# Optimization experiments

Hardware: AMD Instinct MI355X
Metric: run time of the kernel (lower is better)

Reference implementation:

```python
import jax, jax.numpy as jnp
import numpy as np

C = 512
NUM_HEADS = 8
GROUPS = 32
EPS_GN = 1e-5
EPS_ATTN = 1e-6


def setup_inputs() -> dict:
    key = jax.random.key(0)
    ks = jax.random.split(key, 7)
    B, H, W = 8, 64, 64
    x = jax.random.normal(ks[0], (B, C, H, W), dtype=jnp.float32)
    # GroupNorm affine (torch default: weight=1, bias=0)
    norm_gamma = jnp.ones((C,), dtype=jnp.float32)
    norm_beta = jnp.zeros((C,), dtype=jnp.float32)
    # 1x1 conv weights stored as (out, in); torch Conv2d kaiming-ish scale
    qkv_w = jax.random.normal(ks[1], (3 * C, C), dtype=jnp.float32) * (1.0 / np.sqrt(C))
    qkv_b = jax.random.normal(ks[2], (3 * C,), dtype=jnp.float32) * 0.01
    proj_w = jax.random.normal(ks[3], (C, C), dtype=jnp.float32) * (1.0 / np.sqrt(C))
    proj_b = jax.random.normal(ks[4], (C,), dtype=jnp.float32) * 0.01
    return {"x": x, "norm_gamma": norm_gamma, "norm_beta": norm_beta,
            "qkv_w": qkv_w, "qkv_b": qkv_b, "proj_w": proj_w, "proj_b": proj_b}


def _group_norm(x, gamma, beta):
    B, Cc, H, W = x.shape
    xg = x.reshape(B, GROUPS, Cc // GROUPS, H, W)
    mean = xg.mean(axis=(2, 3, 4), keepdims=True)
    var = xg.var(axis=(2, 3, 4), keepdims=True)
    xn = (xg - mean) * jax.lax.rsqrt(var + EPS_GN)
    xn = xn.reshape(B, Cc, H, W)
    return xn * gamma[None, :, None, None] + beta[None, :, None, None]


def reference(x, norm_gamma, norm_beta, qkv_w, qkv_b, proj_w, proj_b):
    B, Cc, H, W = x.shape
    h, d = NUM_HEADS, Cc // NUM_HEADS
    N = H * W
    x_norm = _group_norm(x, norm_gamma, norm_beta)
    # 1x1 conv == channel GEMM
    qkv = jnp.einsum('bchw,oc->bohw', x_norm, qkv_w) + qkv_b[None, :, None, None]
    q, k, v = jnp.split(qkv, 3, axis=1)
    # (B, C, H, W) -> (B, h, N, d)
    def to_heads(t):
        return t.reshape(B, h, d, N).transpose(0, 1, 3, 2)
    q, k, v = to_heads(q), to_heads(k), to_heads(v)
    # phi(x) = elu(x) + 1
    q = jax.nn.elu(q) + 1.0
    k = jax.nn.elu(k) + 1.0
    kv = jnp.einsum('bhnd,bhne->bhde', k, v)          # (B,h,d,d)
    out = jnp.einsum('bhnd,bhde->bhne', q, kv)        # (B,h,N,d)
    denom = jnp.einsum('bhnd,bhd->bhn', q, k.sum(axis=2))
    out = out / (denom[..., None] + EPS_ATTN)
    # (B,h,N,d) -> (B,C,H,W)
    attn = out.transpose(0, 1, 3, 2).reshape(B, Cc, H, W)
    proj = jnp.einsum('bchw,oc->bohw', attn, proj_w) + proj_b[None, :, None, None]
    # dropout is identity at inference
    return x + proj
```

## Files before the change

kernel.cpp:

```cpp
#include <hip/hip_runtime.h>
#include <math.h>

#define BATCH   8
#define CCH     512
#define NHEADS  8
#define HD      64
#define NGROUPS 32
#define CPG     16
#define NSP     4096
#define O1      1536

typedef __attribute__((ext_vector_type(8))) short          short8;
typedef __attribute__((ext_vector_type(8))) unsigned short ushort8;
typedef __attribute__((ext_vector_type(4))) unsigned short ushort4v;
typedef __attribute__((ext_vector_type(4))) float          float4v;

#define GLOAD_LDS16(g, s) __builtin_amdgcn_global_load_lds(                   \
    (const __attribute__((address_space(1))) void*)(g),                       \
    (__attribute__((address_space(3))) void*)(s), 16, 0, 0)

__device__ __forceinline__ float phi_act(float v) {
    return v > 0.f ? v + 1.f : __expf(v);
}
__device__ __forceinline__ unsigned short f2bf(float f) {
    union { float f; unsigned int u; } c; c.f = f;
    unsigned int u = c.u;
    u += 0x7fffu + ((u >> 16) & 1u);
    return (unsigned short)(u >> 16);
}
__device__ __forceinline__ float bf2f(unsigned short s) {
    union { unsigned int u; float f; } c; c.u = ((unsigned int)s) << 16;
    return c.f;
}


__global__ __launch_bounds__(256) void gn_stats(const float* __restrict__ x,
                                                const float* __restrict__ gamma,
                                                const float* __restrict__ beta,
                                                float* __restrict__ ss) {
    const int bg = blockIdx.x;
    const int t  = threadIdx.x;
    const float* base = x + (size_t)bg * (CPG * NSP);
    float s = 0.f, s2 = 0.f;
    #pragma unroll 4
    for (int i = 0; i < 64; ++i) {
        float4 v = *(const float4*)(base + (i * 256 + t) * 4);
        s  += v.x + v.y + v.z + v.w;
        s2 += v.x * v.x + v.y * v.y + v.z * v.z + v.w * v.w;
    }
    __shared__ float r1[256], r2[256];
    r1[t] = s; r2[t] = s2;
    __syncthreads();
    for (int off = 128; off > 0; off >>= 1) {
        if (t < off) { r1[t] += r1[t + off]; r2[t] += r2[t + off]; }
        __syncthreads();
    }
    if (t < CPG) {
        const float inv = 1.f / 65536.f;
        float mean = r1[0] * inv;
        float var  = r2[0] * inv - mean * mean;
        float rstd = rsqrtf(var + 1e-5f);
        int b = bg / NGROUPS, g = bg % NGROUPS;
        int c = g * CPG + t;
        float sc = gamma[c] * rstd;
        float sh = beta[c] - mean * sc;
        ss[(b * CCH + c) * 2]     = sc;
        ss[(b * CCH + c) * 2 + 1] = sh;
    }
}

__global__ __launch_bounds__(256) void conv_w(const float* __restrict__ qw,
                                              const float* __restrict__ pw,
                                              unsigned short* __restrict__ qwb,
                                              unsigned short* __restrict__ pwb,
                                              float* __restrict__ ksum) {
    int i = (blockIdx.x * 256 + threadIdx.x) * 4;
    if (i < O1 * CCH) {
        float4 v = *(const float4*)(qw + i);
        unsigned short o[4] = {f2bf(v.x), f2bf(v.y), f2bf(v.z), f2bf(v.w)};
        *(uint2*)(qwb + i) = *(uint2*)o;
    } else {
        int j = i - O1 * CCH;
        float4 v = *(const float4*)(pw + j);
        unsigned short o[4] = {f2bf(v.x), f2bf(v.y), f2bf(v.z), f2bf(v.w)};
        *(uint2*)(pwb + j) = *(uint2*)o;
    }
    if (blockIdx.x == 0) {
        float4 z = {0.f, 0.f, 0.f, 0.f};
        #pragma unroll
        for (int l = 0; l < 4; ++l)
            *(float4*)(ksum + (l * 256 + threadIdx.x) * 4) = z;
    }
}

__global__ __launch_bounds__(256) void xnT_kernel(const float* __restrict__ x,
                                                  const float* __restrict__ ss,
                                                  unsigned short* __restrict__ xnT) {
    const int n0 = blockIdx.x * 64, c0 = blockIdx.y * 64, b = blockIdx.z;
    const int t = threadIdx.x;
    __shared__ float tile[64][65];
    const float* xb  = x + ((size_t)b * CCH + c0) * NSP + n0;
    const float* ssb = ss + b * CCH * 2;

    const int lr = t / 16, lc = (t % 16) * 4;
    #pragma unroll
    for (int j = 0; j < 4; ++j) {
        int cr = j * 16 + lr;
        float4 v = *(const float4*)(xb + (size_t)cr * NSP + lc);
        float sc = ssb[(c0 + cr) * 2], sh = ssb[(c0 + cr) * 2 + 1];
        tile[cr][lc + 0] = v.x * sc + sh;
        tile[cr][lc + 1] = v.y * sc + sh;
        tile[cr][lc + 2] = v.z * sc + sh;
        tile[cr][lc + 3] = v.w * sc + sh;
    }
    __syncthreads();
    #pragma unroll
    for (int j = 0; j < 2; ++j) {
        int wd = j * 256 + t;
        int n  = wd >> 3;
        int cb = (wd & 7) * 8;
        ushort8 o;
        #pragma unroll
        for (int i = 0; i < 8; ++i) o[i] = f2bf(tile[cb + i][n]);
        *(ushort8*)(xnT + ((size_t)b * NSP + n0 + n) * CCH + c0 + cb) = o;
    }
}

__global__ __launch_bounds__(256) void gemm_q(const unsigned short* __restrict__ A,
                                              const unsigned short* __restrict__ Bt,
                                              const float* __restrict__ bias,
                                              unsigned short* __restrict__ qT) {
    const int n0 = blockIdx.x * 128;
    const int o0 = blockIdx.y * 128;
    const int b  = blockIdx.z;
    const int t  = threadIdx.x;
    const int wv = t >> 6, ln = t & 63;
    const int quad = ln >> 4, lm = ln & 15;
    const int wo = (wv >> 1) * 64, wn = (wv & 1) * 64;

    __shared__ __align__(16) unsigned short As[128 * 64];
    __shared__ __align__(16) unsigned short Bs[128 * 64];

    float4v acc[4][4];
    #pragma unroll
    for (int i = 0; i < 4; ++i)
        #pragma unroll
        for (int j = 0; j < 4; ++j) acc[i][j] = {0.f, 0.f, 0.f, 0.f};

    const unsigned short* aBase = A + (size_t)o0 * CCH;
    const unsigned short* bBase = Bt + ((size_t)b * NSP + n0) * CCH;

    const int srow8 = ln >> 3;
    const int scs   = ((ln & 7) ^ srow8) * 8;
    const int lmp   = (lm & 7);

    for (int k0 = 0; k0 < CCH; k0 += 64) {
        __syncthreads();
        #pragma unroll
        for (int i = 0; i < 4; ++i) {
            int slab = wv + i * 4;
            GLOAD_LDS16(aBase + (size_t)(slab * 8 + srow8) * CCH + k0 + scs,
                        As + slab * 512);
            GLOAD_LDS16(bBase + (size_t)(slab * 8 + srow8) * CCH + k0 + scs,
                        Bs + slab * 512);
        }
        __syncthreads();
        #pragma unroll
        for (int kk = 0; kk < 2; ++kk) {
            const int sc8 = ((kk * 4 + quad) ^ lmp) * 8;
            short8 fw[4], fx[4];
            #pragma unroll
            for (int i = 0; i < 4; ++i)
                fw[i] = *(const short8*)(As + (wo + i * 16 + lm) * 64 + sc8);
            #pragma unroll
            for (int j = 0; j < 4; ++j)
                fx[j] = *(const short8*)(Bs + (wn + j * 16 + lm) * 64 + sc8);
            #pragma unroll
            for (int i = 0; i < 4; ++i)
                #pragma unroll
                for (int j = 0; j < 4; ++j)
                    acc[i][j] = __builtin_amdgcn_mfma_f32_16x16x32_bf16(
                        fw[i], fx[j], acc[i][j], 0, 0, 0);
        }
    }

    #pragma unroll
    for (int i = 0; i < 4; ++i) {
        int ob = o0 + wo + i * 16 + quad * 4;
        float4 b4 = *(const float4*)(bias + ob);
        float bs[4] = {b4.x, b4.y, b4.z, b4.w};
        #pragma unroll
        for (int j = 0; j < 4; ++j) {
            int n = n0 + wn + j * 16 + lm;
            ushort4v pk;
            #pragma unroll
            for (int r = 0; r < 4; ++r)
                pk[r] = f2bf(phi_act(acc[i][j][r] + bs[r]));
            *(ushort4v*)(qT + ((size_t)b * NSP + n) * CCH + ob) = pk;
        }
    }
}

__global__ __launch_bounds__(256) void gemm_kv(const unsigned short* __restrict__ A,
                                               const unsigned short* __restrict__ Bt,
                                               const float* __restrict__ bias,
                                               unsigned short* __restrict__ kb,
                                               unsigned short* __restrict__ vb,
                                               float* __restrict__ ksum) {
    const int n0 = blockIdx.x * 128;
    const int o0 = 512 + blockIdx.y * 128;
    const int b  = blockIdx.z;
    const int t  = threadIdx.x;
    const int wv = t >> 6, ln = t & 63;
    const int quad = ln >> 4, lm = ln & 15;
    const int wo = (wv >> 1) * 64, wn = (wv & 1) * 64;

    __shared__ __align__(16) unsigned short As[128 * 64];
    __shared__ __align__(16) unsigned short Bs[128 * 64];

    float4v acc[4][4];
    #pragma unroll
    for (int i = 0; i < 4; ++i)
        #pragma unroll
        for (int j = 0; j < 4; ++j) acc[i][j] = {0.f, 0.f, 0.f, 0.f};

    const unsigned short* aBase = A + (size_t)o0 * CCH;
    const unsigned short* bBase = Bt + ((size_t)b * NSP + n0) * CCH;

    const int srow8 = ln >> 3;
    const int scs   = ((ln & 7) ^ srow8) * 8;
    const int lmp   = (lm & 7);

    for (int k0 = 0; k0 < CCH; k0 += 64) {
        __syncthreads();
        #pragma unroll
        for (int i = 0; i < 4; ++i) {
            int slab = wv + i * 4;
            GLOAD_LDS16(aBase + (size_t)(slab * 8 + srow8) * CCH + k0 + scs,
                        As + slab * 512);
            GLOAD_LDS16(bBase + (size_t)(slab * 8 + srow8) * CCH + k0 + scs,
                        Bs + slab * 512);
        }
        __syncthreads();
        #pragma unroll
        for (int kk = 0; kk < 2; ++kk) {
            const int sc8 = ((kk * 4 + quad) ^ lmp) * 8;
            short8 fw[4], fx[4];
            #pragma unroll
            for (int i = 0; i < 4; ++i)
                fw[i] = *(const short8*)(As + (wo + i * 16 + lm) * 64 + sc8);
            #pragma unroll
            for (int j = 0; j < 4; ++j)
                fx[j] = *(const short8*)(Bs + (wn + j * 16 + lm) * 64 + sc8);
            #pragma unroll
            for (int i = 0; i < 4; ++i)
                #pragma unroll
                for (int j = 0; j < 4; ++j)
                    acc[i][j] = __builtin_amdgcn_mfma_f32_16x16x32_bf16(
                        fx[j], fw[i], acc[i][j], 0, 0, 0);
        }
    }

    const bool isk = (o0 < 1024);
    unsigned short* dst = isk ? kb : vb;
    const int cb0 = o0 - (isk ? 512 : 1024);
    #pragma unroll
    for (int i = 0; i < 4; ++i) {
        int o = o0 + wo + i * 16 + lm;
        int c = cb0 + wo + i * 16 + lm;
        float bs = bias[o];
        float ksp = 0.f;
        #pragma unroll
        for (int j = 0; j < 4; ++j) {
            int n = n0 + wn + j * 16 + quad * 4;
            ushort4v pk;
            #pragma unroll
            for (int r = 0; r < 4; ++r) {
                float v = acc[i][j][r] + bs;
                if (isk) { v = phi_act(v); ksp += v; }
                pk[r] = f2bf(v);
            }
            *(ushort4v*)(dst + ((size_t)b * CCH + c) * NSP + n) = pk;
        }
        if (isk) {
            ksp += __shfl_xor(ksp, 16);
            ksp += __shfl_xor(ksp, 32);
            if (quad == 0) atomicAdd(ksum + b * CCH + c, ksp);
        }
    }
}

__global__ __launch_bounds__(256) void kv_mfma(const unsigned short* __restrict__ kb,
                                               const unsigned short* __restrict__ vb,
                                               float* __restrict__ kvp) {
    const int chunk = blockIdx.x, bh = blockIdx.y;
    const int b = bh >> 3, h = bh & 7;
    const int t = threadIdx.x;
    const int wv = t >> 6, ln = t & 63;
    const int quad = ln >> 4, lm = ln & 15;
    const int wd = (wv >> 1) * 32, we = (wv & 1) * 32;

    __shared__ __align__(16) unsigned short kt[2 * 64 * 32];
    __shared__ __align__(16) unsigned short vt[2 * 64 * 32];

    float4v acc[2][2];
    #pragma unroll
    for (int i = 0; i < 2; ++i)
        #pragma unroll
        for (int j = 0; j < 2; ++j) acc[i][j] = {0.f, 0.f, 0.f, 0.f};

    const unsigned short* kbase = kb + ((size_t)b * CCH + h * 64) * NSP + chunk * 1024;
    const unsigned short* vbase = vb + ((size_t)b * CCH + h * 64) * NSP + chunk * 1024;
    const int srow = ln >> 2;
    const int scs  = ((ln & 3) ^ ((ln >> 3) & 3)) * 8;
    const int sc8  = (quad ^ ((lm >> 1) & 3)) * 8;

    for (int it = 0; it < 16; ++it) {
        int noff = it * 64;
        __syncthreads();
        GLOAD_LDS16(kbase + (size_t)(wv * 16 + srow) * NSP + noff + scs,      kt + wv * 512);
        GLOAD_LDS16(kbase + (size_t)(wv * 16 + srow) * NSP + noff + 32 + scs, kt + 2048 + wv * 512);
        GLOAD_LDS16(vbase + (size_t)(wv * 16 + srow) * NSP + noff + scs,      vt + wv * 512);
        GLOAD_LDS16(vbase + (size_t)(wv * 16 + srow) * NSP + noff + 32 + scs, vt + 2048 + wv * 512);
        __syncthreads();
        #pragma unroll
        for (int kk = 0; kk < 2; ++kk) {
            short8 a0 = *(const short8*)(kt + kk * 2048 + (wd + lm) * 32 + sc8);
            short8 a1 = *(const short8*)(kt + kk * 2048 + (wd + 16 + lm) * 32 + sc8);
            short8 b0 = *(const short8*)(vt + kk * 2048 + (we + lm) * 32 + sc8);
            short8 b1 = *(const short8*)(vt + kk * 2048 + (we + 16 + lm) * 32 + sc8);
            acc[0][0] = __builtin_amdgcn_mfma_f32_16x16x32_bf16(a0, b0, acc[0][0], 0, 0, 0);
            acc[0][1] = __builtin_amdgcn_mfma_f32_16x16x32_bf16(a0, b1, acc[0][1], 0, 0, 0);
            acc[1][0] = __builtin_amdgcn_mfma_f32_16x16x32_bf16(a1, b0, acc[1][0], 0, 0, 0);
            acc[1][1] = __builtin_amdgcn_mfma_f32_16x16x32_bf16(a1, b1, acc[1][1], 0, 0, 0);
        }
    }
    #pragma unroll
    for (int i = 0; i < 2; ++i)
        #pragma unroll
        for (int j = 0; j < 2; ++j) {
            int e = we + j * 16 + lm;
            int d = wd + i * 16 + quad * 4;
            float4 r = {acc[i][j][0], acc[i][j][1], acc[i][j][2], acc[i][j][3]};
            *(float4*)(kvp + ((size_t)(chunk * 64 + bh) * 64 + e) * 64 + d) = r;
        }
}

__global__ __launch_bounds__(256) void kv_reduce(const float* __restrict__ kvp,
                                                 unsigned short* __restrict__ kvTb) {
    int idx4 = (blockIdx.x * 256 + threadIdx.x) * 4;
    float4 s = {0.f, 0.f, 0.f, 0.f};
    #pragma unroll
    for (int p = 0; p < 4; ++p) {
        float4 v = *(const float4*)(kvp + (size_t)p * (64 * 64 * 64) + idx4);
        s.x += v.x; s.y += v.y; s.z += v.z; s.w += v.w;
    }
    ushort4v o = {f2bf(s.x), f2bf(s.y), f2bf(s.z), f2bf(s.w)};
    *(ushort4v*)(kvTb + idx4) = o;
}

__global__ __launch_bounds__(256) void attn_mfma(const unsigned short* __restrict__ qT,
                                                 const unsigned short* __restrict__ kvTb,
                                                 const float* __restrict__ ksum,
                                                 unsigned short* __restrict__ attnT) {
    const int n0 = blockIdx.x * 256;
    const int bh = blockIdx.y;
    const int b = bh >> 3, h = bh & 7;
    const int t = threadIdx.x;
    const int wv = t >> 6, ln = t & 63;
    const int quad = ln >> 4, lm = ln & 15;
    const int nb = n0 + wv * 64;

    __shared__ __align__(16) unsigned short kvs[64 * 72];
    __shared__ float kss[64];

    #pragma unroll
    for (int l = 0; l < 2; ++l) {
        int ch = l * 256 + t;
        int e = ch >> 3, c8 = ch & 7;
        *(ushort8*)(kvs + e * 72 + c8 * 8) =
            *(const ushort8*)(kvTb + (size_t)bh * 4096 + ch * 8);
    }
    if (t < 64) kss[t] = ksum[b * CCH + h * 64 + t];
    __syncthreads();

    short8 bq[4][2];
    #pragma unroll
    for (int j = 0; j < 4; ++j)
        #pragma unroll
        for (int kk = 0; kk < 2; ++kk) {
            int n = nb + j * 16 + lm;
            bq[j][kk] = *(const short8*)(qT + ((size_t)b * NSP + n) * CCH +
                                         h * 64 + kk * 32 + quad * 8);
        }
    short8 ak[4][2];
    #pragma unroll
    for (int i = 0; i < 4; ++i)
        #pragma unroll
        for (int kk = 0; kk < 2; ++kk)
            ak[i][kk] = *(const short8*)(kvs + (i * 16 + lm) * 72 + kk * 32 + quad * 8);

    float4v acc[4][4];
    #pragma unroll
    for (int i = 0; i < 4; ++i)
        #pragma unroll
        for (int j = 0; j < 4; ++j) acc[i][j] = {0.f, 0.f, 0.f, 0.f};
    #pragma unroll
    for (int kk = 0; kk < 2; ++kk)
        #pragma unroll
        for (int i = 0; i < 4; ++i)
            #pragma unroll
            for (int j = 0; j < 4; ++j)
                acc[i][j] = __builtin_amdgcn_mfma_f32_16x16x32_bf16(
                    ak[i][kk], bq[j][kk], acc[i][j], 0, 0, 0);

    float rden[4];
    #pragma unroll
    for (int j = 0; j < 4; ++j) {
        float dp = 0.f;
        #pragma unroll
        for (int kk = 0; kk < 2; ++kk)
            #pragma unroll
            for (int l = 0; l < 8; ++l)
                dp += bf2f((unsigned short)bq[j][kk][l]) * kss[kk * 32 + quad * 8 + l];
        dp += __shfl_xor(dp, 16);
        dp += __shfl_xor(dp, 32);
        rden[j] = 1.f / (dp + 1e-6f);
    }

    #pragma unroll
    for (int i = 0; i < 4; ++i) {
        int e = i * 16 + quad * 4;
        #pragma unroll
        for (int j = 0; j < 4; ++j) {
            int n = nb + j * 16 + lm;
            ushort4v pk;
            #pragma unroll
            for (int r = 0; r < 4; ++r)
                pk[r] = f2bf(acc[i][j][r] * rden[j]);
            *(ushort4v*)(attnT + ((size_t)b * NSP + n) * CCH + h * 64 + e) = pk;
        }
    }
}

__global__ __launch_bounds__(256) void gemm_proj(const unsigned short* __restrict__ A,
                                                 const unsigned short* __restrict__ Bt,
                                                 const float* __restrict__ bias,
                                                 const float* __restrict__ resid,
                                                 float* __restrict__ outF) {
    const int n0 = blockIdx.x * 128;
    const int o0 = blockIdx.y * 128;
    const int b  = blockIdx.z;
    const int t  = threadIdx.x;
    const int wv = t >> 6, ln = t & 63;
    const int quad = ln >> 4, lm = ln & 15;
    const int wo = (wv >> 1) * 64, wn = (wv & 1) * 64;

    __shared__ __align__(16) unsigned short As[128 * 64];
    __shared__ __align__(16) unsigned short Bs[128 * 64];

    float4v acc[4][4];
    #pragma unroll
    for (int i = 0; i < 4; ++i)
        #pragma unroll
        for (int j = 0; j < 4; ++j) acc[i][j] = {0.f, 0.f, 0.f, 0.f};

    const unsigned short* aBase = A + (size_t)o0 * CCH;
    const unsigned short* bBase = Bt + ((size_t)b * NSP + n0) * CCH;

    const int srow8 = ln >> 3;
    const int scs   = ((ln & 7) ^ srow8) * 8;
    const int lmp   = (lm & 7);

    for (int k0 = 0; k0 < CCH; k0 += 64) {
        __syncthreads();
        #pragma unroll
        for (int i = 0; i < 4; ++i) {
            int slab = wv + i * 4;
            GLOAD_LDS16(aBase + (size_t)(slab * 8 + srow8) * CCH + k0 + scs,
                        As + slab * 512);
            GLOAD_LDS16(bBase + (size_t)(slab * 8 + srow8) * CCH + k0 + scs,
                        Bs + slab * 512);
        }
        __syncthreads();
        #pragma unroll
        for (int kk = 0; kk < 2; ++kk) {
            const int sc8 = ((kk * 4 + quad) ^ lmp) * 8;
            short8 fw[4], fx[4];
            #pragma unroll
            for (int i = 0; i < 4; ++i)
                fw[i] = *(const short8*)(As + (wo + i * 16 + lm) * 64 + sc8);
            #pragma unroll
            for (int j = 0; j < 4; ++j)
                fx[j] = *(const short8*)(Bs + (wn + j * 16 + lm) * 64 + sc8);
            #pragma unroll
            for (int i = 0; i < 4; ++i)
                #pragma unroll
                for (int j = 0; j < 4; ++j)
                    acc[i][j] = __builtin_amdgcn_mfma_f32_16x16x32_bf16(
                        fx[j], fw[i], acc[i][j], 0, 0, 0);
        }
    }

    #pragma unroll
    for (int i = 0; i < 4; ++i) {
        int o = o0 + wo + i * 16 + lm;
        float bs = bias[o];
        #pragma unroll
        for (int j = 0; j < 4; ++j) {
            int n = n0 + wn + j * 16 + quad * 4;
            size_t off = ((size_t)b * CCH + o) * NSP + n;
            float4 rv = *(const float4*)(resid + off);
            float4 w = {acc[i][j][0] + bs + rv.x, acc[i][j][1] + bs + rv.y,
                        acc[i][j][2] + bs + rv.z, acc[i][j][3] + bs + rv.w};
            *(float4*)(outF + off) = w;
        }
    }
}

extern "C" void kernel_launch(void* const* d_in, const int* in_sizes, int n_in,
                              void* d_out, int out_size, void* d_ws, size_t ws_size,
                              hipStream_t stream) {
    const float* x      = (const float*)d_in[0];
    const float* gamma  = (const float*)d_in[1];
    const float* beta   = (const float*)d_in[2];
    const float* qkv_w  = (const float*)d_in[3];
    const float* qkv_b  = (const float*)d_in[4];
    const float* proj_w = (const float*)d_in[5];
    const float* proj_b = (const float*)d_in[6];
    float* out = (float*)d_out;

    float* ws   = (float*)d_ws;
    float* ss   = ws;
    float* ksum = ss + 8192;
    float* kvp  = ksum + 4096;
    unsigned short* xnT   = (unsigned short*)(kvp + 4 * 64 * 64 * 64);
    unsigned short* qT    = xnT + (size_t)BATCH * NSP * CCH;
    unsigned short* kb    = qT  + (size_t)BATCH * NSP * CCH;
    unsigned short* vb    = kb  + (size_t)BATCH * NSP * CCH;
    unsigned short* attnT = vb  + (size_t)BATCH * NSP * CCH;
    unsigned short* kvTb  = attnT + (size_t)BATCH * NSP * CCH;
    unsigned short* wqb   = kvTb + (size_t)64 * 64 * 64;
    unsigned short* wpb   = wqb + (size_t)O1 * CCH;

    gn_stats<<<BATCH * NGROUPS, 256, 0, stream>>>(x, gamma, beta, ss);
    conv_w<<<(O1 * CCH + CCH * CCH) / 4 / 256, 256, 0, stream>>>(qkv_w, proj_w, wqb, wpb, ksum);
    xnT_kernel<<<dim3(NSP / 64, CCH / 64, BATCH), 256, 0, stream>>>(x, ss, xnT);

    gemm_q <<<dim3(NSP / 128, 4, BATCH), 256, 0, stream>>>(wqb, xnT, qkv_b, qT);
    gemm_kv<<<dim3(NSP / 128, 8, BATCH), 256, 0, stream>>>(wqb, xnT, qkv_b, kb, vb, ksum);

    kv_mfma<<<dim3(4, 64), 256, 0, stream>>>(kb, vb, kvp);
    kv_reduce<<<256, 256, 0, stream>>>(kvp, kvTb);
    attn_mfma<<<dim3(NSP / 256, 64), 256, 0, stream>>>(qT, kvTb, ksum, attnT);

    gemm_proj<<<dim3(NSP / 128, CCH / 128, BATCH), 256, 0, stream>>>(
        wpb, attnT, proj_b, x, out);
}
```

Baseline: 295.9 us.

## Widen QKV GEMM tiles and compute key sums via MFMA in kv kernel

The q and kv projection GEMMs now use 128x256 output tiles instead of 128x128, so each weight tile loaded into LDS is reused across twice as many spatial columns. The per-channel key sum no longer uses atomics in the gemm_kv epilogue; kv_mfma computes it with extra MFMAs against a ones vector, and kv_reduce sums the partials, which also removes the zero-init in conv_w. In exchange the larger tiles double accumulator registers and LDS use, which may lower occupancy, and the key sum is now taken over bf16-rounded values.

```diff
diff --git a/kernel.cpp b/kernel.cpp
--- a/kernel.cpp
+++ b/kernel.cpp
@@ -72,8 +72,7 @@
 __global__ __launch_bounds__(256) void conv_w(const float* __restrict__ qw,
                                               const float* __restrict__ pw,
                                               unsigned short* __restrict__ qwb,
-                                              unsigned short* __restrict__ pwb,
-                                              float* __restrict__ ksum) {
+                                              unsigned short* __restrict__ pwb) {
     int i = (blockIdx.x * 256 + threadIdx.x) * 4;
     if (i < O1 * CCH) {
         float4 v = *(const float4*)(qw + i);
@@ -85,12 +84,6 @@
         unsigned short o[4] = {f2bf(v.x), f2bf(v.y), f2bf(v.z), f2bf(v.w)};
         *(uint2*)(pwb + j) = *(uint2*)o;
     }
-    if (blockIdx.x == 0) {
-        float4 z = {0.f, 0.f, 0.f, 0.f};
-        #pragma unroll
-        for (int l = 0; l < 4; ++l)
-            *(float4*)(ksum + (l * 256 + threadIdx.x) * 4) = z;
-    }
 }
 
 __global__ __launch_bounds__(256) void xnT_kernel(const float* __restrict__ x,
@@ -130,22 +123,22 @@
                                               const unsigned short* __restrict__ Bt,
                                               const float* __restrict__ bias,
                                               unsigned short* __restrict__ qT) {
-    const int n0 = blockIdx.x * 128;
+    const int n0 = blockIdx.x * 256;
     const int o0 = blockIdx.y * 128;
     const int b  = blockIdx.z;
     const int t  = threadIdx.x;
     const int wv = t >> 6, ln = t & 63;
     const int quad = ln >> 4, lm = ln & 15;
-    const int wo = (wv >> 1) * 64, wn = (wv & 1) * 64;
+    const int wo = (wv >> 1) * 64, wn = (wv & 1) * 128;
 
     __shared__ __align__(16) unsigned short As[128 * 64];
-    __shared__ __align__(16) unsigned short Bs[128 * 64];
-
-    float4v acc[4][4];
+    __shared__ __align__(16) unsigned short Bs[256 * 64];
+
+    float4v acc[4][8];
     #pragma unroll
     for (int i = 0; i < 4; ++i)
         #pragma unroll
-        for (int j = 0; j < 4; ++j) acc[i][j] = {0.f, 0.f, 0.f, 0.f};
+        for (int j = 0; j < 8; ++j) acc[i][j] = {0.f, 0.f, 0.f, 0.f};
 
     const unsigned short* aBase = A + (size_t)o0 * CCH;
     const unsigned short* bBase = Bt + ((size_t)b * NSP + n0) * CCH;
@@ -158,27 +151,31 @@
         __syncthreads();
         #pragma unroll
         for (int i = 0; i < 4; ++i) {
-            int slab = wv + i * 4;
-            GLOAD_LDS16(aBase + (size_t)(slab * 8 + srow8) * CCH + k0 + scs,
-                        As + slab * 512);
-            GLOAD_LDS16(bBase + (size_t)(slab * 8 + srow8) * CCH + k0 + scs,
-                        Bs + slab * 512);
+            int s = wv + i * 4;
+            GLOAD_LDS16(aBase + (size_t)(s * 8 + srow8) * CCH + k0 + scs,
+                        As + s * 512);
+        }
+        #pragma unroll
+        for (int i = 0; i < 8; ++i) {
+            int s = wv + i * 4;
+            GLOAD_LDS16(bBase + (size_t)(s * 8 + srow8) * CCH + k0 + scs,
+                        Bs + s * 512);
         }
         __syncthreads();
         #pragma unroll
         for (int kk = 0; kk < 2; ++kk) {
             const int sc8 = ((kk * 4 + quad) ^ lmp) * 8;
-            short8 fw[4], fx[4];
+            short8 fw[4], fx[8];
             #pragma unroll
             for (int i = 0; i < 4; ++i)
                 fw[i] = *(const short8*)(As + (wo + i * 16 + lm) * 64 + sc8);
             #pragma unroll
-            for (int j = 0; j < 4; ++j)
+            for (int j = 0; j < 8; ++j)
                 fx[j] = *(const short8*)(Bs + (wn + j * 16 + lm) * 64 + sc8);
             #pragma unroll
             for (int i = 0; i < 4; ++i)
                 #pragma unroll
-                for (int j = 0; j < 4; ++j)
+                for (int j = 0; j < 8; ++j)
                     acc[i][j] = __builtin_amdgcn_mfma_f32_16x16x32_bf16(
                         fw[i], fx[j], acc[i][j], 0, 0, 0);
         }
@@ -190,7 +187,7 @@
         float4 b4 = *(const float4*)(bias + ob);
         float bs[4] = {b4.x, b4.y, b4.z, b4.w};
         #pragma unroll
-        for (int j = 0; j < 4; ++j) {
+        for (int j = 0; j < 8; ++j) {
             int n = n0 + wn + j * 16 + lm;
             ushort4v pk;
             #pragma unroll
@@ -205,24 +202,23 @@
                                                const unsigned short* __restrict__ Bt,
                                                const float* __restrict__ bias,
                                                unsigned short* __restrict__ kb,
-                                               unsigned short* __restrict__ vb,
-                                               float* __restrict__ ksum) {
-    const int n0 = blockIdx.x * 128;
+                                               unsigned short* __restrict__ vb) {
+    const int n0 = blockIdx.x * 256;
     const int o0 = 512 + blockIdx.y * 128;
     const int b  = blockIdx.z;
     const int t  = threadIdx.x;
     const int wv = t >> 6, ln = t & 63;
     const int quad = ln >> 4, lm = ln & 15;
-    const int wo = (wv >> 1) * 64, wn = (wv & 1) * 64;
+    const int wo = (wv >> 1) * 64, wn = (wv & 1) * 128;
 
     __shared__ __align__(16) unsigned short As[128 * 64];
-    __shared__ __align__(16) unsigned short Bs[128 * 64];
-
-    float4v acc[4][4];
+    __shared__ __align__(16) unsigned short Bs[256 * 64];
+
+    float4v acc[4][8];
     #pragma unroll
     for (int i = 0; i < 4; ++i)
         #pragma unroll
-        for (int j = 0; j < 4; ++j) acc[i][j] = {0.f, 0.f, 0.f, 0.f};
+        for (int j = 0; j < 8; ++j) acc[i][j] = {0.f, 0.f, 0.f, 0.f};
 
     const unsigned short* aBase = A + (size_t)o0 * CCH;
     const unsigned short* bBase = Bt + ((size_t)b * NSP + n0) * CCH;
@@ -235,27 +231,31 @@
         __syncthreads();
         #pragma unroll
         for (int i = 0; i < 4; ++i) {
-            int slab = wv + i * 4;
-            GLOAD_LDS16(aBase + (size_t)(slab * 8 + srow8) * CCH + k0 + scs,
-                        As + slab * 512);
-            GLOAD_LDS16(bBase + (size_t)(slab * 8 + srow8) * CCH + k0 + scs,
-                        Bs + slab * 512);
+            int s = wv + i * 4;
+            GLOAD_LDS16(aBase + (size_t)(s * 8 + srow8) * CCH + k0 + scs,
+                        As + s * 512);
+        }
+        #pragma unroll
+        for (int i = 0; i < 8; ++i) {
+            int s = wv + i * 4;
+            GLOAD_LDS16(bBase + (size_t)(s * 8 + srow8) * CCH + k0 + scs,
+                        Bs + s * 512);
         }
         __syncthreads();
         #pragma unroll
         for (int kk = 0; kk < 2; ++kk) {
             const int sc8 = ((kk * 4 + quad) ^ lmp) * 8;
-            short8 fw[4], fx[4];
+            short8 fw[4], fx[8];
             #pragma unroll
             for (int i = 0; i < 4; ++i)
                 fw[i] = *(const short8*)(As + (wo + i * 16 + lm) * 64 + sc8);
             #pragma unroll
-            for (int j = 0; j < 4; ++j)
+            for (int j = 0; j < 8; ++j)
                 fx[j] = *(const short8*)(Bs + (wn + j * 16 + lm) * 64 + sc8);
             #pragma unroll
             for (int i = 0; i < 4; ++i)
                 #pragma unroll
-                for (int j = 0; j < 4; ++j)
+                for (int j = 0; j < 8; ++j)
                     acc[i][j] = __builtin_amdgcn_mfma_f32_16x16x32_bf16(
                         fx[j], fw[i], acc[i][j], 0, 0, 0);
         }
@@ -263,36 +263,31 @@
 
     const bool isk = (o0 < 1024);
     unsigned short* dst = isk ? kb : vb;
-    const int cb0 = o0 - (isk ? 512 : 1024);
+    const int coff = isk ? 512 : 1024;
     #pragma unroll
     for (int i = 0; i < 4; ++i) {
         int o = o0 + wo + i * 16 + lm;
-        int c = cb0 + wo + i * 16 + lm;
+        int c = o - coff;
         float bs = bias[o];
-        float ksp = 0.f;
-        #pragma unroll
-        for (int j = 0; j < 4; ++j) {
+        #pragma unroll
+        for (int j = 0; j < 8; ++j) {
             int n = n0 + wn + j * 16 + quad * 4;
             ushort4v pk;
             #pragma unroll
             for (int r = 0; r < 4; ++r) {
                 float v = acc[i][j][r] + bs;
-                if (isk) { v = phi_act(v); ksp += v; }
+                if (isk) v = phi_act(v);
                 pk[r] = f2bf(v);
             }
             *(ushort4v*)(dst + ((size_t)b * CCH + c) * NSP + n) = pk;
         }
-        if (isk) {
-            ksp += __shfl_xor(ksp, 16);
-            ksp += __shfl_xor(ksp, 32);
-            if (quad == 0) atomicAdd(ksum + b * CCH + c, ksp);
-        }
     }
 }
 
 __global__ __launch_bounds__(256) void kv_mfma(const unsigned short* __restrict__ kb,
                                                const unsigned short* __restrict__ vb,
-                                               float* __restrict__ kvp) {
+                                               float* __restrict__ kvp,
+                                               float* __restrict__ ksp) {
     const int chunk = blockIdx.x, bh = blockIdx.y;
     const int b = bh >> 3, h = bh & 7;
     const int t = threadIdx.x;
@@ -308,6 +303,11 @@
     for (int i = 0; i < 2; ++i)
         #pragma unroll
         for (int j = 0; j < 2; ++j) acc[i][j] = {0.f, 0.f, 0.f, 0.f};
+    float4v ks0 = {0.f, 0.f, 0.f, 0.f}, ks1 = {0.f, 0.f, 0.f, 0.f};
+
+    short8 ones;
+    #pragma unroll
+    for (int l = 0; l < 8; ++l) ones[l] = (short)0x3F80;
 
     const unsigned short* kbase = kb + ((size_t)b * CCH + h * 64) * NSP + chunk * 1024;
     const unsigned short* vbase = vb + ((size_t)b * CCH + h * 64) * NSP + chunk * 1024;
@@ -333,6 +333,8 @@
             acc[0][1] = __builtin_amdgcn_mfma_f32_16x16x32_bf16(a0, b1, acc[0][1], 0, 0, 0);
             acc[1][0] = __builtin_amdgcn_mfma_f32_16x16x32_bf16(a1, b0, acc[1][0], 0, 0, 0);
             acc[1][1] = __builtin_amdgcn_mfma_f32_16x16x32_bf16(a1, b1, acc[1][1], 0, 0, 0);
+            ks0 = __builtin_amdgcn_mfma_f32_16x16x32_bf16(a0, ones, ks0, 0, 0, 0);
+            ks1 = __builtin_amdgcn_mfma_f32_16x16x32_bf16(a1, ones, ks1, 0, 0, 0);
         }
     }
     #pragma unroll
@@ -344,24 +346,45 @@
             float4 r = {acc[i][j][0], acc[i][j][1], acc[i][j][2], acc[i][j][3]};
             *(float4*)(kvp + ((size_t)(chunk * 64 + bh) * 64 + e) * 64 + d) = r;
         }
+    if ((wv & 1) == 0 && lm == 0) {
+        float* kd = ksp + (size_t)(chunk * 64 + bh) * 64;
+        float4 r0 = {ks0[0], ks0[1], ks0[2], ks0[3]};
+        float4 r1 = {ks1[0], ks1[1], ks1[2], ks1[3]};
+        *(float4*)(kd + wd + quad * 4)      = r0;
+        *(float4*)(kd + wd + 16 + quad * 4) = r1;
+    }
 }
 
 __global__ __launch_bounds__(256) void kv_reduce(const float* __restrict__ kvp,
-                                                 unsigned short* __restrict__ kvTb) {
+                                                 const float* __restrict__ ksp,
+                                                 unsigned short* __restrict__ kvTb,
+                                                 float* __restrict__ ksf) {
+    const int NKV = 64 * 64 * 64;
     int idx4 = (blockIdx.x * 256 + threadIdx.x) * 4;
-    float4 s = {0.f, 0.f, 0.f, 0.f};
-    #pragma unroll
-    for (int p = 0; p < 4; ++p) {
-        float4 v = *(const float4*)(kvp + (size_t)p * (64 * 64 * 64) + idx4);
-        s.x += v.x; s.y += v.y; s.z += v.z; s.w += v.w;
-    }
-    ushort4v o = {f2bf(s.x), f2bf(s.y), f2bf(s.z), f2bf(s.w)};
-    *(ushort4v*)(kvTb + idx4) = o;
+    if (idx4 < NKV) {
+        float4 s = {0.f, 0.f, 0.f, 0.f};
+        #pragma unroll
+        for (int p = 0; p < 4; ++p) {
+            float4 v = *(const float4*)(kvp + (size_t)p * NKV + idx4);
+            s.x += v.x; s.y += v.y; s.z += v.z; s.w += v.w;
+        }
+        ushort4v o = {f2bf(s.x), f2bf(s.y), f2bf(s.z), f2bf(s.w)};
+        *(ushort4v*)(kvTb + idx4) = o;
+    } else if (idx4 - NKV < 64 * 64) {
+        int i2 = idx4 - NKV;
+        float4 s = {0.f, 0.f, 0.f, 0.f};
+        #pragma unroll
+        for (int p = 0; p < 4; ++p) {
+            float4 v = *(const float4*)(ksp + p * 4096 + i2);
+            s.x += v.x; s.y += v.y; s.z += v.z; s.w += v.w;
+        }
+        *(float4*)(ksf + i2) = s;
+    }
 }
 
 __global__ __launch_bounds__(256) void attn_mfma(const unsigned short* __restrict__ qT,
                                                  const unsigned short* __restrict__ kvTb,
-                                                 const float* __restrict__ ksum,
+                                                 const float* __restrict__ ksf,
                                                  unsigned short* __restrict__ attnT) {
     const int n0 = blockIdx.x * 256;
     const int bh = blockIdx.y;
@@ -381,7 +404,7 @@
         *(ushort8*)(kvs + e * 72 + c8 * 8) =
             *(const ushort8*)(kvTb + (size_t)bh * 4096 + ch * 8);
     }
-    if (t < 64) kss[t] = ksum[b * CCH + h * 64 + t];
+    if (t < 64) kss[t] = ksf[bh * 64 + t];
     __syncthreads();
 
     short8 bq[4][2];
@@ -532,9 +555,10 @@
 
     float* ws   = (float*)d_ws;
     float* ss   = ws;
-    float* ksum = ss + 8192;
-    float* kvp  = ksum + 4096;
-    unsigned short* xnT   = (unsigned short*)(kvp + 4 * 64 * 64 * 64);
+    float* kvp  = ss + 8192;
+    float* ksp  = kvp + 4 * 64 * 64 * 64;
+    float* ksf  = ksp + 4 * 64 * 64;
+    unsigned short* xnT   = (unsigned short*)(ksf + 64 * 64);
     unsigned short* qT    = xnT + (size_t)BATCH * NSP * CCH;
     unsigned short* kb    = qT  + (size_t)BATCH * NSP * CCH;
     unsigned short* vb    = kb  + (size_t)BATCH * NSP * CCH;
@@ -544,15 +568,15 @@
     unsigned short* wpb   = wqb + (size_t)O1 * CCH;
 
     gn_stats<<<BATCH * NGROUPS, 256, 0, stream>>>(x, gamma, beta, ss);
-    conv_w<<<(O1 * CCH + CCH * CCH) / 4 / 256, 256, 0, stream>>>(qkv_w, proj_w, wqb, wpb, ksum);
+    conv_w<<<(O1 * CCH + CCH * CCH) / 4 / 256, 256, 0, stream>>>(qkv_w, proj_w, wqb, wpb);
     xnT_kernel<<<dim3(NSP / 64, CCH / 64, BATCH), 256, 0, stream>>>(x, ss, xnT);
 
-    gemm_q <<<dim3(NSP / 128, 4, BATCH), 256, 0, stream>>>(wqb, xnT, qkv_b, qT);
-    gemm_kv<<<dim3(NSP / 128, 8, BATCH), 256, 0, stream>>>(wqb, xnT, qkv_b, kb, vb, ksum);
-
-    kv_mfma<<<dim3(4, 64), 256, 0, stream>>>(kb, vb, kvp);
-    kv_reduce<<<256, 256, 0, stream>>>(kvp, kvTb);
-    attn_mfma<<<dim3(NSP / 256, 64), 256, 0, stream>>>(qT, kvTb, ksum, attnT);
+    gemm_q <<<dim3(NSP / 256, 4, BATCH), 256, 0, stream>>>(wqb, xnT, qkv_b, qT);
+    gemm_kv<<<dim3(NSP / 256, 8, BATCH), 256, 0, stream>>>(wqb, xnT, qkv_b, kb, vb);
+
+    kv_mfma<<<dim3(4, 64), 256, 0, stream>>>(kb, vb, kvp, ksp);
+    kv_reduce<<<(64 * 64 * 64 + 64 * 64) / 4 / 256, 256, 0, stream>>>(kvp, ksp, kvTb, ksf);
+    attn_mfma<<<dim3(NSP / 256, 64), 256, 0, stream>>>(qT, kvTb, ksf, attnT);
 
     gemm_proj<<<dim3(NSP / 128, CCH / 128, BATCH), 256, 0, stream>>>(
         wpb, attnT, proj_b, x, out);
```

After: 325.8 us. +10.1%, slower.
